# Performance work log

Measured on AMD Instinct MI355X. Metric: run time of the kernel, lower is better.

The kernel has to match this reference:

```python
import jax, jax.numpy as jnp
import numpy as np

B, F, K, D = 512, 2048, 64, 16


def setup_inputs() -> dict:
    key = jax.random.key(0)
    k1, k2 = jax.random.split(key)
    x = jax.random.normal(k1, (B, F), dtype=jnp.float32)
    # glorot-uniform-ish init for the projection kernel [F, K, D]
    limit = np.sqrt(6.0 / (F + K * D)).astype(np.float32)
    kernel = jax.random.uniform(k2, (F, K, D), dtype=jnp.float32, minval=-limit, maxval=limit)
    return {"x": x, "kernel": kernel}


def reference(x, kernel):
    # activation: [B, K, D]
    act = jnp.einsum('bf,fkd->bkd', x, kernel)
    # pairwise L1 distance over D: diffs [B, K, D, B] -> abs_diffs [B, K, B]
    diffs = act[:, :, :, None] - jnp.transpose(act, (1, 2, 0))[None, :, :, :]
    abs_diffs = jnp.sum(jnp.abs(diffs), axis=2)
    # exp-similarity summed over the other batch elements (includes self: +1)
    feats = jnp.sum(jnp.exp(-abs_diffs), axis=2)  # [B, K]
    return jnp.concatenate([x, feats], axis=1)  # [B, F + K]
```

## Files before the change

kernel.cpp:

```cpp
#include <hip/hip_runtime.h>

#define B_   512
#define F_   2048
#define K_   64
#define D_   16
#define N_   1024
#define OUTW (F_+K_)
#define LOG2E 1.44269504088896340736f

typedef __attribute__((ext_vector_type(8))) short short8;
typedef __attribute__((ext_vector_type(4))) float f32x4;

__device__ __forceinline__ ushort f2bf(float f) {
    union { float f; unsigned u; } un; un.f = f;
    unsigned u = un.u;
    u += 0x7FFF + ((u >> 16) & 1);
    return (ushort)(u >> 16);
}

__device__ __forceinline__ float exp2_neg(float x) {
    float r;
    asm("v_exp_f32 %0, -%1" : "=v"(r) : "v"(x));
    return r;
}

__global__ __launch_bounds__(256) void convert_x_kernel(const float* __restrict__ x,
                                                        float* __restrict__ out,
                                                        ushort* __restrict__ xb) {
    const int i = blockIdx.x * 256 + threadIdx.x;
    float4 v = ((const float4*)x)[i];
    const int b = i >> 9, c = i & 511;
    ((float4*)out)[b * (OUTW / 4) + c] = v;
    ushort4 u = make_ushort4(f2bf(v.x * LOG2E), f2bf(v.y * LOG2E),
                             f2bf(v.z * LOG2E), f2bf(v.w * LOG2E));
    ((ushort4*)xb)[i] = u;
}

__global__ __launch_bounds__(256) void convert_wt_kernel(const float* __restrict__ w,
                                                         ushort* __restrict__ wt) {
    __shared__ float t[32][33];
    const int f0 = blockIdx.x * 32;
    const int n0 = blockIdx.y * 32;
    const int tid = threadIdx.x;
    const int r = tid >> 3;
    const int c4 = (tid & 7) * 4;
    float4 v = *(const float4*)(w + (size_t)(f0 + r) * N_ + n0 + c4);
    t[r][c4 + 0] = v.x; t[r][c4 + 1] = v.y; t[r][c4 + 2] = v.z; t[r][c4 + 3] = v.w;
    __syncthreads();
    ushort4 u = make_ushort4(f2bf(t[c4 + 0][r]), f2bf(t[c4 + 1][r]),
                             f2bf(t[c4 + 2][r]), f2bf(t[c4 + 3][r]));
    *(ushort4*)(wt + (size_t)(n0 + r) * F_ + f0 + c4) = u;
}

__global__ __launch_bounds__(256) void gemm_mfma_kernel(const ushort* __restrict__ xb,
                                                        const ushort* __restrict__ wt,
                                                        float* __restrict__ act) {
    const int bm0 = blockIdx.x * 64;
    const int bn0 = blockIdx.y * 32;
    const int tid = threadIdx.x;
    const int l   = tid & 63;
    const int w   = tid >> 6;
    const int mw  = (w >> 1) * 32;
    const int nw  = (w & 1) * 16;
    const int lr  = l & 15;
    const int lk  = (l >> 4) * 8;

    const ushort* pa0 = xb + (size_t)(bm0 + mw + lr) * F_ + lk;
    const ushort* pa1 = pa0 + 16 * F_;
    const ushort* pb0 = wt + (size_t)(bn0 + nw + lr) * F_ + lk;

    f32x4 acc0 = {}, acc1 = {};

    #pragma unroll 4
    for (int kk = 0; kk < F_; kk += 32) {
        short8 a0 = *(const short8*)(pa0 + kk);
        short8 a1 = *(const short8*)(pa1 + kk);
        short8 b0 = *(const short8*)(pb0 + kk);
        acc0 = __builtin_amdgcn_mfma_f32_16x16x32_bf16(a0, b0, acc0, 0, 0, 0);
        acc1 = __builtin_amdgcn_mfma_f32_16x16x32_bf16(a1, b0, acc1, 0, 0, 0);
    }

    const int n = bn0 + nw + lr;
    const int k = n >> 4, d = n & 15;
    const int mbase = bm0 + mw + (l >> 4) * 4;
    float* dst = act + (size_t)k * (B_ * D_) + d;
    #pragma unroll
    for (int r = 0; r < 4; ++r) {
        dst[(size_t)(mbase + r) * D_]      = acc0[r];
        dst[(size_t)(mbase + 16 + r) * D_] = acc1[r];
    }
}

__global__ __launch_bounds__(512) void pairwise_kernel(const float* __restrict__ act,
                                                       float* __restrict__ out) {
    __shared__ float s_act[B_ * D_];
    __shared__ float red[8][64];

    const int bt = blockIdx.x;
    const int k  = blockIdx.y;
    const int tid  = threadIdx.x;
    const int lane = tid & 63;
    const int wave = tid >> 6;

    const float4* src = (const float4*)(act + (size_t)k * (B_ * D_));
    #pragma unroll
    for (int i = 0; i < 4; ++i)
        ((float4*)s_act)[tid + i * 512] = src[tid + i * 512];
    __syncthreads();

    const int b = bt * 64 + lane;
    const float4* arow = (const float4*)&s_act[b * D_];
    const float4 a0 = arow[0], a1 = arow[1], a2 = arow[2], a3 = arow[3];

    float p0 = 0.0f, p1 = 0.0f;
    const int b2lo = wave * 64;
    #pragma unroll 2
    for (int b2 = b2lo; b2 < b2lo + 64; b2 += 2) {
        {
            const float4* v = (const float4*)&s_act[b2 * D_];
            const float4 v0 = v[0], v1 = v[1], v2 = v[2], v3 = v[3];
            float t0 = fabsf(a0.x - v0.x) + fabsf(a0.y - v0.y);
            float t1 = fabsf(a0.z - v0.z) + fabsf(a0.w - v0.w);
            float t2 = fabsf(a1.x - v1.x) + fabsf(a1.y - v1.y);
            float t3 = fabsf(a1.z - v1.z) + fabsf(a1.w - v1.w);
            float t4 = fabsf(a2.x - v2.x) + fabsf(a2.y - v2.y);
            float t5 = fabsf(a2.z - v2.z) + fabsf(a2.w - v2.w);
            float t6 = fabsf(a3.x - v3.x) + fabsf(a3.y - v3.y);
            float t7 = fabsf(a3.z - v3.z) + fabsf(a3.w - v3.w);
            float s = ((t0 + t1) + (t2 + t3)) + ((t4 + t5) + (t6 + t7));
            p0 += exp2_neg(s);
        }
        {
            const float4* v = (const float4*)&s_act[(b2 + 1) * D_];
            const float4 v0 = v[0], v1 = v[1], v2 = v[2], v3 = v[3];
            float t0 = fabsf(a0.x - v0.x) + fabsf(a0.y - v0.y);
            float t1 = fabsf(a0.z - v0.z) + fabsf(a0.w - v0.w);
            float t2 = fabsf(a1.x - v1.x) + fabsf(a1.y - v1.y);
            float t3 = fabsf(a1.z - v1.z) + fabsf(a1.w - v1.w);
            float t4 = fabsf(a2.x - v2.x) + fabsf(a2.y - v2.y);
            float t5 = fabsf(a2.z - v2.z) + fabsf(a2.w - v2.w);
            float t6 = fabsf(a3.x - v3.x) + fabsf(a3.y - v3.y);
            float t7 = fabsf(a3.z - v3.z) + fabsf(a3.w - v3.w);
            float s = ((t0 + t1) + (t2 + t3)) + ((t4 + t5) + (t6 + t7));
            p1 += exp2_neg(s);
        }
    }

    red[wave][lane] = p0 + p1;
    __syncthreads();
    if (wave == 0) {
        float total = 0.0f;
        #pragma unroll
        for (int i = 0; i < 8; ++i) total += red[i][lane];
        out[(size_t)b * OUTW + F_ + k] = total;
    }
}

extern "C" void kernel_launch(void* const* d_in, const int* in_sizes, int n_in,
                              void* d_out, int out_size, void* d_ws, size_t ws_size,
                              hipStream_t stream) {
    const float* x = (const float*)d_in[0];
    const float* wsrc = (const float*)d_in[1];
    float* out = (float*)d_out;

    ushort* xb  = (ushort*)d_ws;
    ushort* wt  = (ushort*)((char*)d_ws + (size_t)2 * 1024 * 1024);
    float*  act = (float*)((char*)d_ws + (size_t)6 * 1024 * 1024);

    convert_x_kernel<<<1024, 256, 0, stream>>>(x, out, xb);
    convert_wt_kernel<<<dim3(64, 32), 256, 0, stream>>>(wsrc, wt);
    gemm_mfma_kernel<<<dim3(8, 32), 256, 0, stream>>>(xb, wt, act);
    pairwise_kernel<<<dim3(8, K_), 512, 0, stream>>>(act, out);
}
```

Before: 112.5 us.

## Fuse all four stages into one cooperative kernel with grid syncs

Merges the x conversion, weight transpose/convert, MFMA GEMM and pairwise-distance stages into a single cooperative kernel of 256 blocks x 512 threads, separated by grid.sync barriers. The goal is to remove three kernel launch gaps and their per-launch overhead. The GEMM now splits K across two wave groups and reduces the partial sums through LDS. The pairwise stage loops over two units per block. The cost is that only 256 blocks are resident, fewer than the 1024, 2048 and 512 blocks the separate kernels used, and grid-wide barriers add their own sync latency.

```diff
diff --git a/kernel.cpp b/kernel.cpp
--- a/kernel.cpp
+++ b/kernel.cpp
@@ -1,4 +1,7 @@
 #include <hip/hip_runtime.h>
+#include <hip/hip_cooperative_groups.h>
+
+namespace cg = cooperative_groups;
 
 #define B_   512
 #define F_   2048
@@ -24,135 +27,168 @@
     return r;
 }
 
-__global__ __launch_bounds__(256) void convert_x_kernel(const float* __restrict__ x,
-                                                        float* __restrict__ out,
-                                                        ushort* __restrict__ xb) {
-    const int i = blockIdx.x * 256 + threadIdx.x;
-    float4 v = ((const float4*)x)[i];
-    const int b = i >> 9, c = i & 511;
-    ((float4*)out)[b * (OUTW / 4) + c] = v;
-    ushort4 u = make_ushort4(f2bf(v.x * LOG2E), f2bf(v.y * LOG2E),
-                             f2bf(v.z * LOG2E), f2bf(v.w * LOG2E));
-    ((ushort4*)xb)[i] = u;
-}
-
-__global__ __launch_bounds__(256) void convert_wt_kernel(const float* __restrict__ w,
-                                                         ushort* __restrict__ wt) {
-    __shared__ float t[32][33];
-    const int f0 = blockIdx.x * 32;
-    const int n0 = blockIdx.y * 32;
+__global__ __launch_bounds__(512) void fused_kernel(const float* __restrict__ x,
+                                                    const float* __restrict__ w,
+                                                    float* __restrict__ out,
+                                                    ushort* __restrict__ xb,
+                                                    ushort* __restrict__ wt,
+                                                    float* __restrict__ act) {
+    __shared__ float lds[8192 + 512];
     const int tid = threadIdx.x;
-    const int r = tid >> 3;
-    const int c4 = (tid & 7) * 4;
-    float4 v = *(const float4*)(w + (size_t)(f0 + r) * N_ + n0 + c4);
-    t[r][c4 + 0] = v.x; t[r][c4 + 1] = v.y; t[r][c4 + 2] = v.z; t[r][c4 + 3] = v.w;
-    __syncthreads();
-    ushort4 u = make_ushort4(f2bf(t[c4 + 0][r]), f2bf(t[c4 + 1][r]),
-                             f2bf(t[c4 + 2][r]), f2bf(t[c4 + 3][r]));
-    *(ushort4*)(wt + (size_t)(n0 + r) * F_ + f0 + c4) = u;
-}
-
-__global__ __launch_bounds__(256) void gemm_mfma_kernel(const ushort* __restrict__ xb,
-                                                        const ushort* __restrict__ wt,
-                                                        float* __restrict__ act) {
-    const int bm0 = blockIdx.x * 64;
-    const int bn0 = blockIdx.y * 32;
-    const int tid = threadIdx.x;
-    const int l   = tid & 63;
-    const int w   = tid >> 6;
-    const int mw  = (w >> 1) * 32;
-    const int nw  = (w & 1) * 16;
-    const int lr  = l & 15;
-    const int lk  = (l >> 4) * 8;
-
-    const ushort* pa0 = xb + (size_t)(bm0 + mw + lr) * F_ + lk;
-    const ushort* pa1 = pa0 + 16 * F_;
-    const ushort* pb0 = wt + (size_t)(bn0 + nw + lr) * F_ + lk;
-
-    f32x4 acc0 = {}, acc1 = {};
-
-    #pragma unroll 4
-    for (int kk = 0; kk < F_; kk += 32) {
-        short8 a0 = *(const short8*)(pa0 + kk);
-        short8 a1 = *(const short8*)(pa1 + kk);
-        short8 b0 = *(const short8*)(pb0 + kk);
-        acc0 = __builtin_amdgcn_mfma_f32_16x16x32_bf16(a0, b0, acc0, 0, 0, 0);
-        acc1 = __builtin_amdgcn_mfma_f32_16x16x32_bf16(a1, b0, acc1, 0, 0, 0);
-    }
-
-    const int n = bn0 + nw + lr;
-    const int k = n >> 4, d = n & 15;
-    const int mbase = bm0 + mw + (l >> 4) * 4;
-    float* dst = act + (size_t)k * (B_ * D_) + d;
-    #pragma unroll
-    for (int r = 0; r < 4; ++r) {
-        dst[(size_t)(mbase + r) * D_]      = acc0[r];
-        dst[(size_t)(mbase + 16 + r) * D_] = acc1[r];
-    }
-}
-
-__global__ __launch_bounds__(512) void pairwise_kernel(const float* __restrict__ act,
-                                                       float* __restrict__ out) {
-    __shared__ float s_act[B_ * D_];
-    __shared__ float red[8][64];
-
-    const int bt = blockIdx.x;
-    const int k  = blockIdx.y;
-    const int tid  = threadIdx.x;
-    const int lane = tid & 63;
-    const int wave = tid >> 6;
-
-    const float4* src = (const float4*)(act + (size_t)k * (B_ * D_));
-    #pragma unroll
-    for (int i = 0; i < 4; ++i)
-        ((float4*)s_act)[tid + i * 512] = src[tid + i * 512];
-    __syncthreads();
-
-    const int b = bt * 64 + lane;
-    const float4* arow = (const float4*)&s_act[b * D_];
-    const float4 a0 = arow[0], a1 = arow[1], a2 = arow[2], a3 = arow[3];
-
-    float p0 = 0.0f, p1 = 0.0f;
-    const int b2lo = wave * 64;
-    #pragma unroll 2
-    for (int b2 = b2lo; b2 < b2lo + 64; b2 += 2) {
-        {
-            const float4* v = (const float4*)&s_act[b2 * D_];
-            const float4 v0 = v[0], v1 = v[1], v2 = v[2], v3 = v[3];
-            float t0 = fabsf(a0.x - v0.x) + fabsf(a0.y - v0.y);
-            float t1 = fabsf(a0.z - v0.z) + fabsf(a0.w - v0.w);
-            float t2 = fabsf(a1.x - v1.x) + fabsf(a1.y - v1.y);
-            float t3 = fabsf(a1.z - v1.z) + fabsf(a1.w - v1.w);
-            float t4 = fabsf(a2.x - v2.x) + fabsf(a2.y - v2.y);
-            float t5 = fabsf(a2.z - v2.z) + fabsf(a2.w - v2.w);
-            float t6 = fabsf(a3.x - v3.x) + fabsf(a3.y - v3.y);
-            float t7 = fabsf(a3.z - v3.z) + fabsf(a3.w - v3.w);
-            float s = ((t0 + t1) + (t2 + t3)) + ((t4 + t5) + (t6 + t7));
-            p0 += exp2_neg(s);
-        }
-        {
-            const float4* v = (const float4*)&s_act[(b2 + 1) * D_];
-            const float4 v0 = v[0], v1 = v[1], v2 = v[2], v3 = v[3];
-            float t0 = fabsf(a0.x - v0.x) + fabsf(a0.y - v0.y);
-            float t1 = fabsf(a0.z - v0.z) + fabsf(a0.w - v0.w);
-            float t2 = fabsf(a1.x - v1.x) + fabsf(a1.y - v1.y);
-            float t3 = fabsf(a1.z - v1.z) + fabsf(a1.w - v1.w);
-            float t4 = fabsf(a2.x - v2.x) + fabsf(a2.y - v2.y);
-            float t5 = fabsf(a2.z - v2.z) + fabsf(a2.w - v2.w);
-            float t6 = fabsf(a3.x - v3.x) + fabsf(a3.y - v3.y);
-            float t7 = fabsf(a3.z - v3.z) + fabsf(a3.w - v3.w);
-            float s = ((t0 + t1) + (t2 + t3)) + ((t4 + t5) + (t6 + t7));
-            p1 += exp2_neg(s);
-        }
-    }
-
-    red[wave][lane] = p0 + p1;
-    __syncthreads();
-    if (wave == 0) {
-        float total = 0.0f;
+    const int blk = blockIdx.x;
+    cg::grid_group grid = cg::this_grid();
+
+    {
+        const int base = blk * 512 + tid;
         #pragma unroll
-        for (int i = 0; i < 8; ++i) total += red[i][lane];
-        out[(size_t)b * OUTW + F_ + k] = total;
+        for (int i = 0; i < 2; ++i) {
+            const int idx = base + i * 131072;
+            float4 v = ((const float4*)x)[idx];
+            const int b = idx >> 9, c = idx & 511;
+            ((float4*)out)[b * (OUTW / 4) + c] = v;
+            ushort4 u = make_ushort4(f2bf(v.x * LOG2E), f2bf(v.y * LOG2E),
+                                     f2bf(v.z * LOG2E), f2bf(v.w * LOG2E));
+            ((ushort4*)xb)[idx] = u;
+        }
+    }
+    {
+        float (*t)[33] = (float(*)[33])lds;
+        const int r  = tid >> 4;
+        const int c2 = (tid & 15) * 2;
+        float2 vv[8];
+        #pragma unroll
+        for (int i = 0; i < 8; ++i) {
+            const int tile = blk * 8 + i;
+            vv[i] = *(const float2*)(w + (size_t)((tile >> 5) * 32 + r) * N_ + (tile & 31) * 32 + c2);
+        }
+        #pragma unroll
+        for (int i = 0; i < 8; ++i) {
+            const int tile = blk * 8 + i;
+            const int f0 = (tile >> 5) * 32, n0 = (tile & 31) * 32;
+            __syncthreads();
+            t[r][c2] = vv[i].x; t[r][c2 + 1] = vv[i].y;
+            __syncthreads();
+            ushort2 u = make_ushort2(f2bf(t[c2][r]), f2bf(t[c2 + 1][r]));
+            *(ushort2*)(wt + (size_t)(n0 + r) * F_ + f0 + c2) = u;
+        }
+    }
+    grid.sync();
+
+    {
+        const int l  = tid & 63;
+        const int wv = tid >> 6;
+        const int bm0 = (blk >> 5) * 64;
+        const int bn0 = (blk & 31) * 32;
+        const int mw = ((wv >> 1) & 1) * 32;
+        const int nw = (wv & 1) * 16;
+        const int khalf = (wv >> 2) * 1024;
+        const int lr = l & 15;
+        const int lk = (l >> 4) * 8;
+
+        const ushort* pa0 = xb + (size_t)(bm0 + mw + lr) * F_ + khalf + lk;
+        const ushort* pa1 = pa0 + 16 * F_;
+        const ushort* pb0 = wt + (size_t)(bn0 + nw + lr) * F_ + khalf + lk;
+
+        f32x4 acc0 = {}, acc1 = {};
+        #pragma unroll 4
+        for (int kk = 0; kk < 1024; kk += 32) {
+            short8 a0 = *(const short8*)(pa0 + kk);
+            short8 a1 = *(const short8*)(pa1 + kk);
+            short8 b0 = *(const short8*)(pb0 + kk);
+            acc0 = __builtin_amdgcn_mfma_f32_16x16x32_bf16(a0, b0, acc0, 0, 0, 0);
+            acc1 = __builtin_amdgcn_mfma_f32_16x16x32_bf16(a1, b0, acc1, 0, 0, 0);
+        }
+
+        if (wv >= 4) {
+            #pragma unroll
+            for (int j = 0; j < 4; ++j) {
+                lds[(((wv - 4) * 8 + j) * 64) + l]     = acc0[j];
+                lds[(((wv - 4) * 8 + j + 4) * 64) + l] = acc1[j];
+            }
+        }
+        __syncthreads();
+        if (wv < 4) {
+            #pragma unroll
+            for (int j = 0; j < 4; ++j) {
+                acc0[j] += lds[((wv * 8 + j) * 64) + l];
+                acc1[j] += lds[((wv * 8 + j + 4) * 64) + l];
+            }
+            const int n = bn0 + nw + lr;
+            const int k = n >> 4, d = n & 15;
+            const int mbase = bm0 + mw + (l >> 4) * 4;
+            float* dst = act + (size_t)k * (B_ * D_) + d;
+            #pragma unroll
+            for (int r = 0; r < 4; ++r) {
+                dst[(size_t)(mbase + r) * D_]      = acc0[r];
+                dst[(size_t)(mbase + 16 + r) * D_] = acc1[r];
+            }
+        }
+    }
+    grid.sync();
+
+    {
+        const int lane = tid & 63;
+        const int wv   = tid >> 6;
+        float* s_act = lds;
+        float* red   = lds + 8192;
+        #pragma unroll 1
+        for (int half = 0; half < 2; ++half) {
+            const int u  = blk + half * 256;
+            const int bt = u & 7, k = u >> 3;
+            __syncthreads();
+            const float4* src = (const float4*)(act + (size_t)k * (B_ * D_));
+            #pragma unroll
+            for (int i = 0; i < 4; ++i)
+                ((float4*)s_act)[tid + i * 512] = src[tid + i * 512];
+            __syncthreads();
+
+            const int b = bt * 64 + lane;
+            const float4* arow = (const float4*)&s_act[b * D_];
+            const float4 a0 = arow[0], a1 = arow[1], a2 = arow[2], a3 = arow[3];
+
+            float p0 = 0.0f, p1 = 0.0f;
+            const int b2lo = wv * 64;
+            #pragma unroll 2
+            for (int b2 = b2lo; b2 < b2lo + 64; b2 += 2) {
+                {
+                    const float4* v = (const float4*)&s_act[b2 * D_];
+                    const float4 v0 = v[0], v1 = v[1], v2 = v[2], v3 = v[3];
+                    float t0 = fabsf(a0.x - v0.x) + fabsf(a0.y - v0.y);
+                    float t1 = fabsf(a0.z - v0.z) + fabsf(a0.w - v0.w);
+                    float t2 = fabsf(a1.x - v1.x) + fabsf(a1.y - v1.y);
+                    float t3 = fabsf(a1.z - v1.z) + fabsf(a1.w - v1.w);
+                    float t4 = fabsf(a2.x - v2.x) + fabsf(a2.y - v2.y);
+                    float t5 = fabsf(a2.z - v2.z) + fabsf(a2.w - v2.w);
+                    float t6 = fabsf(a3.x - v3.x) + fabsf(a3.y - v3.y);
+                    float t7 = fabsf(a3.z - v3.z) + fabsf(a3.w - v3.w);
+                    float s = ((t0 + t1) + (t2 + t3)) + ((t4 + t5) + (t6 + t7));
+                    p0 += exp2_neg(s);
+                }
+                {
+                    const float4* v = (const float4*)&s_act[(b2 + 1) * D_];
+                    const float4 v0 = v[0], v1 = v[1], v2 = v[2], v3 = v[3];
+                    float t0 = fabsf(a0.x - v0.x) + fabsf(a0.y - v0.y);
+                    float t1 = fabsf(a0.z - v0.z) + fabsf(a0.w - v0.w);
+                    float t2 = fabsf(a1.x - v1.x) + fabsf(a1.y - v1.y);
+                    float t3 = fabsf(a1.z - v1.z) + fabsf(a1.w - v1.w);
+                    float t4 = fabsf(a2.x - v2.x) + fabsf(a2.y - v2.y);
+                    float t5 = fabsf(a2.z - v2.z) + fabsf(a2.w - v2.w);
+                    float t6 = fabsf(a3.x - v3.x) + fabsf(a3.y - v3.y);
+                    float t7 = fabsf(a3.z - v3.z) + fabsf(a3.w - v3.w);
+                    float s = ((t0 + t1) + (t2 + t3)) + ((t4 + t5) + (t6 + t7));
+                    p1 += exp2_neg(s);
+                }
+            }
+
+            red[wv * 64 + lane] = p0 + p1;
+            __syncthreads();
+            if (wv == 0) {
+                float total = 0.0f;
+                #pragma unroll
+                for (int i = 0; i < 8; ++i) total += red[i * 64 + lane];
+                out[(size_t)b * OUTW + F_ + k] = total;
+            }
+        }
     }
 }
 
@@ -167,8 +203,6 @@
     ushort* wt  = (ushort*)((char*)d_ws + (size_t)2 * 1024 * 1024);
     float*  act = (float*)((char*)d_ws + (size_t)6 * 1024 * 1024);
 
-    convert_x_kernel<<<1024, 256, 0, stream>>>(x, out, xb);
-    convert_wt_kernel<<<dim3(64, 32), 256, 0, stream>>>(wsrc, wt);
-    gemm_mfma_kernel<<<dim3(8, 32), 256, 0, stream>>>(xb, wt, act);
-    pairwise_kernel<<<dim3(8, K_), 512, 0, stream>>>(act, out);
-}
+    void* args[] = {(void*)&x, (void*)&wsrc, (void*)&out, (void*)&xb, (void*)&wt, (void*)&act};
+    hipLaunchCooperativeKernel((const void*)fused_kernel, dim3(256), dim3(512), args, 0, stream);
+}
```

Result: slower. 173.7 us (+54.4%).

## Merge conversion kernels and split GEMM over K with partial-sum reduction

Applied to the files above, without the earlier changes.

Fuses the x and weight conversion kernels into a single launch, with each weight-transpose block now processing 8 tiles. The GEMM is split four ways along the F reduction dimension (grid z=4), so it launches 1024 blocks instead of 256 and fills more CUs. Each split writes its own partial activation buffer, and the pairwise kernel sums the four partials while loading into shared memory. This removes one launch and raises GEMM parallelism, at the cost of four times the activation writes and reads, plus extra workspace.

```diff
diff --git a/kernel.cpp b/kernel.cpp
--- a/kernel.cpp
+++ b/kernel.cpp
@@ -24,39 +24,47 @@
     return r;
 }
 
-__global__ __launch_bounds__(256) void convert_x_kernel(const float* __restrict__ x,
-                                                        float* __restrict__ out,
-                                                        ushort* __restrict__ xb) {
-    const int i = blockIdx.x * 256 + threadIdx.x;
-    float4 v = ((const float4*)x)[i];
-    const int b = i >> 9, c = i & 511;
-    ((float4*)out)[b * (OUTW / 4) + c] = v;
-    ushort4 u = make_ushort4(f2bf(v.x * LOG2E), f2bf(v.y * LOG2E),
-                             f2bf(v.z * LOG2E), f2bf(v.w * LOG2E));
-    ((ushort4*)xb)[i] = u;
-}
-
-__global__ __launch_bounds__(256) void convert_wt_kernel(const float* __restrict__ w,
-                                                         ushort* __restrict__ wt) {
+__global__ __launch_bounds__(256) void prep_kernel(const float* __restrict__ x,
+                                                   const float* __restrict__ w,
+                                                   float* __restrict__ out,
+                                                   ushort* __restrict__ xb,
+                                                   ushort* __restrict__ wt) {
     __shared__ float t[32][33];
-    const int f0 = blockIdx.x * 32;
-    const int n0 = blockIdx.y * 32;
+    const int blk = blockIdx.x;
     const int tid = threadIdx.x;
-    const int r = tid >> 3;
-    const int c4 = (tid & 7) * 4;
-    float4 v = *(const float4*)(w + (size_t)(f0 + r) * N_ + n0 + c4);
-    t[r][c4 + 0] = v.x; t[r][c4 + 1] = v.y; t[r][c4 + 2] = v.z; t[r][c4 + 3] = v.w;
-    __syncthreads();
-    ushort4 u = make_ushort4(f2bf(t[c4 + 0][r]), f2bf(t[c4 + 1][r]),
-                             f2bf(t[c4 + 2][r]), f2bf(t[c4 + 3][r]));
-    *(ushort4*)(wt + (size_t)(n0 + r) * F_ + f0 + c4) = u;
+    if (blk < 1024) {
+        const int i = blk * 256 + tid;
+        float4 v = ((const float4*)x)[i];
+        const int b = i >> 9, c = i & 511;
+        ((float4*)out)[b * (OUTW / 4) + c] = v;
+        ushort4 u = make_ushort4(f2bf(v.x * LOG2E), f2bf(v.y * LOG2E),
+                                 f2bf(v.z * LOG2E), f2bf(v.w * LOG2E));
+        ((ushort4*)xb)[i] = u;
+    } else {
+        const int r  = tid >> 3;
+        const int c4 = (tid & 7) * 4;
+        #pragma unroll 1
+        for (int i = 0; i < 8; ++i) {
+            const int tb = (blk - 1024) * 8 + i;
+            const int f0 = (tb >> 5) * 32, n0 = (tb & 31) * 32;
+            float4 v = *(const float4*)(w + (size_t)(f0 + r) * N_ + n0 + c4);
+            __syncthreads();
+            t[r][c4 + 0] = v.x; t[r][c4 + 1] = v.y;
+            t[r][c4 + 2] = v.z; t[r][c4 + 3] = v.w;
+            __syncthreads();
+            ushort4 u = make_ushort4(f2bf(t[c4 + 0][r]), f2bf(t[c4 + 1][r]),
+                                     f2bf(t[c4 + 2][r]), f2bf(t[c4 + 3][r]));
+            *(ushort4*)(wt + (size_t)(n0 + r) * F_ + f0 + c4) = u;
+        }
+    }
 }
 
 __global__ __launch_bounds__(256) void gemm_mfma_kernel(const ushort* __restrict__ xb,
                                                         const ushort* __restrict__ wt,
-                                                        float* __restrict__ act) {
+                                                        float* __restrict__ actp) {
     const int bm0 = blockIdx.x * 64;
     const int bn0 = blockIdx.y * 32;
+    const int f0  = blockIdx.z * 512;
     const int tid = threadIdx.x;
     const int l   = tid & 63;
     const int w   = tid >> 6;
@@ -65,14 +73,13 @@
     const int lr  = l & 15;
     const int lk  = (l >> 4) * 8;
 
-    const ushort* pa0 = xb + (size_t)(bm0 + mw + lr) * F_ + lk;
+    const ushort* pa0 = xb + (size_t)(bm0 + mw + lr) * F_ + f0 + lk;
     const ushort* pa1 = pa0 + 16 * F_;
-    const ushort* pb0 = wt + (size_t)(bn0 + nw + lr) * F_ + lk;
+    const ushort* pb0 = wt + (size_t)(bn0 + nw + lr) * F_ + f0 + lk;
 
     f32x4 acc0 = {}, acc1 = {};
-
     #pragma unroll 4
-    for (int kk = 0; kk < F_; kk += 32) {
+    for (int kk = 0; kk < 512; kk += 32) {
         short8 a0 = *(const short8*)(pa0 + kk);
         short8 a1 = *(const short8*)(pa1 + kk);
         short8 b0 = *(const short8*)(pb0 + kk);
@@ -83,7 +90,7 @@
     const int n = bn0 + nw + lr;
     const int k = n >> 4, d = n & 15;
     const int mbase = bm0 + mw + (l >> 4) * 4;
-    float* dst = act + (size_t)k * (B_ * D_) + d;
+    float* dst = actp + (size_t)blockIdx.z * (K_ * B_ * D_) + (size_t)k * (B_ * D_) + d;
     #pragma unroll
     for (int r = 0; r < 4; ++r) {
         dst[(size_t)(mbase + r) * D_]      = acc0[r];
@@ -91,7 +98,7 @@
     }
 }
 
-__global__ __launch_bounds__(512) void pairwise_kernel(const float* __restrict__ act,
+__global__ __launch_bounds__(512) void pairwise_kernel(const float* __restrict__ actp,
                                                        float* __restrict__ out) {
     __shared__ float s_act[B_ * D_];
     __shared__ float red[8][64];
@@ -102,17 +109,22 @@
     const int lane = tid & 63;
     const int wave = tid >> 6;
 
-    const float4* src = (const float4*)(act + (size_t)k * (B_ * D_));
+    const f32x4* p0 = (const f32x4*)(actp + (size_t)k * (B_ * D_));
+    const f32x4* p1 = p0 + (K_ * B_ * D_) / 4;
+    const f32x4* p2 = p1 + (K_ * B_ * D_) / 4;
+    const f32x4* p3 = p2 + (K_ * B_ * D_) / 4;
     #pragma unroll
-    for (int i = 0; i < 4; ++i)
-        ((float4*)s_act)[tid + i * 512] = src[tid + i * 512];
+    for (int i = 0; i < 4; ++i) {
+        const int idx = tid + i * 512;
+        ((f32x4*)s_act)[idx] = (p0[idx] + p1[idx]) + (p2[idx] + p3[idx]);
+    }
     __syncthreads();
 
     const int b = bt * 64 + lane;
     const float4* arow = (const float4*)&s_act[b * D_];
     const float4 a0 = arow[0], a1 = arow[1], a2 = arow[2], a3 = arow[3];
 
-    float p0 = 0.0f, p1 = 0.0f;
+    float p0a = 0.0f, p1a = 0.0f;
     const int b2lo = wave * 64;
     #pragma unroll 2
     for (int b2 = b2lo; b2 < b2lo + 64; b2 += 2) {
@@ -128,7 +140,7 @@
             float t6 = fabsf(a3.x - v3.x) + fabsf(a3.y - v3.y);
             float t7 = fabsf(a3.z - v3.z) + fabsf(a3.w - v3.w);
             float s = ((t0 + t1) + (t2 + t3)) + ((t4 + t5) + (t6 + t7));
-            p0 += exp2_neg(s);
+            p0a += exp2_neg(s);
         }
         {
             const float4* v = (const float4*)&s_act[(b2 + 1) * D_];
@@ -142,11 +154,11 @@
             float t6 = fabsf(a3.x - v3.x) + fabsf(a3.y - v3.y);
             float t7 = fabsf(a3.z - v3.z) + fabsf(a3.w - v3.w);
             float s = ((t0 + t1) + (t2 + t3)) + ((t4 + t5) + (t6 + t7));
-            p1 += exp2_neg(s);
+            p1a += exp2_neg(s);
         }
     }
 
-    red[wave][lane] = p0 + p1;
+    red[wave][lane] = p0a + p1a;
     __syncthreads();
     if (wave == 0) {
         float total = 0.0f;
@@ -163,12 +175,11 @@
     const float* wsrc = (const float*)d_in[1];
     float* out = (float*)d_out;
 
-    ushort* xb  = (ushort*)d_ws;
-    ushort* wt  = (ushort*)((char*)d_ws + (size_t)2 * 1024 * 1024);
-    float*  act = (float*)((char*)d_ws + (size_t)6 * 1024 * 1024);
+    ushort* xb   = (ushort*)d_ws;
+    ushort* wt   = (ushort*)((char*)d_ws + (size_t)2 * 1024 * 1024);
+    float*  actp = (float*)((char*)d_ws + (size_t)6 * 1024 * 1024);
 
-    convert_x_kernel<<<1024, 256, 0, stream>>>(x, out, xb);
-    convert_wt_kernel<<<dim3(64, 32), 256, 0, stream>>>(wsrc, wt);
-    gemm_mfma_kernel<<<dim3(8, 32), 256, 0, stream>>>(xb, wt, act);
-    pairwise_kernel<<<dim3(8, K_), 512, 0, stream>>>(act, out);
+    prep_kernel<<<1280, 256, 0, stream>>>(x, wsrc, out, xb, wt);
+    gemm_mfma_kernel<<<dim3(8, 32, 4), 256, 0, stream>>>(xb, wt, actp);
+    pairwise_kernel<<<dim3(8, K_), 512, 0, stream>>>(actp, out);
 }
```

After: 120.6 us. 7.2% more time.
